# Kernel optimization log

Hardware: AMD Instinct MI355X
Metric: run time of the kernel (lower is better)

Reference implementation:

```python
import jax, jax.numpy as jnp
import numpy as np

N = 500000   # num_nodes
B = 512      # batch_size
D = 128      # node_dim
G = 128      # global_dim
MC = 64      # max_cubes
M = 24       # max_moves_per_cube
H = 128      # MLP hidden
NEG = -1000000000.0


def setup_inputs() -> dict:
    key = jax.random.key(0)
    ks = jax.random.split(key, 8)
    node_features = jax.random.normal(ks[0], (N, D), jnp.float32)
    global_features = jax.random.normal(ks[1], (B, G), jnp.float32)
    cube_mask = jax.random.randint(ks[2], (N,), 0, 2) == 1
    batch = jnp.sort(jax.random.randint(ks[3], (N,), 0, B))
    move_mask = jax.random.randint(ks[4], (B, MC, M), 0, 2) == 1
    W1 = jax.random.normal(ks[5], (D + G, H), jnp.float32) * 0.05
    b1 = jnp.zeros((H,), jnp.float32)
    W2 = jax.random.normal(ks[6], (H, M), jnp.float32) * 0.05
    b2 = jnp.zeros((M,), jnp.float32)
    return {"node_features": node_features, "global_features": global_features,
            "W1": W1, "b1": b1, "W2": W2, "b2": b2,
            "cube_mask": cube_mask, "batch": batch, "move_mask": move_mask}


def reference(node_features, global_features, W1, b1, W2, b2, cube_mask, batch, move_mask):
    bsz = global_features.shape[0]
    max_cubes, moves = move_mask.shape[1], move_mask.shape[2]
    batch = batch.astype(jnp.int32)

    # gather global features per node, concat, small MLP (scores computed for all
    # nodes; only cube-node rows are ever scattered, matching the original math)
    combined = jnp.concatenate([node_features, global_features[batch]], axis=-1)  # [N, D+G]
    h = jax.nn.relu(combined @ W1 + b1)                                           # [N, H]
    scores = h @ W2 + b2                                                          # [N, M]

    # per-batch cumulative cube count (batch is sorted): cube_idx_in_batch
    mask_i = cube_mask.astype(jnp.int32)
    cum = jnp.cumsum(mask_i)                                   # inclusive prefix count of cubes
    counts = jax.ops.segment_sum(mask_i, batch, num_segments=bsz)
    offsets = jnp.concatenate([jnp.zeros((1,), jnp.int32),
                               jnp.cumsum(counts)[:-1].astype(jnp.int32)])
    cube_idx = cum - 1 - offsets[batch]                        # index of cube within its graph

    valid = cube_mask & (cube_idx < max_cubes)
    ib = jnp.where(valid, batch, bsz)      # out-of-range rows -> dropped
    ic = jnp.where(valid, cube_idx, 0)

    logits = jnp.full((bsz, max_cubes, moves), NEG, dtype=scores.dtype)
    logits = logits.at[ib, ic].set(scores, mode="drop")        # unique (ib, ic) per valid node

    logits_flat = logits.reshape(bsz, -1)
    logits_flat = jnp.where(move_mask.reshape(bsz, -1), logits_flat, NEG)
    return logits_flat
```

## Files before the change

### kernel.cpp

```cpp
#include <hip/hip_runtime.h>

typedef short bf16x8 __attribute__((ext_vector_type(8)));
typedef float f32x4 __attribute__((ext_vector_type(4)));

#define NEGV -1000000000.0f

__device__ __forceinline__ unsigned short f2bf(float f) {
    unsigned int u = __float_as_uint(f);
    u += 0x7FFFu + ((u >> 16) & 1u);
    return (unsigned short)(u >> 16);
}

__global__ void prep_kernel(const float* __restrict__ W1, const float* __restrict__ W2,
                            const int* __restrict__ batch, int N, int B,
                            int* __restrict__ batch_start,
                            unsigned short* __restrict__ w1t, unsigned short* __restrict__ w2t) {
    int idx = blockIdx.x * 256 + threadIdx.x;
    if (idx < N) {
        int bcur = batch[idx];
        if (idx == 0) {
            for (int bb = 0; bb <= bcur; ++bb) batch_start[bb] = 0;
        } else {
            int bprev = batch[idx - 1];
            for (int bb = bprev + 1; bb <= bcur; ++bb) batch_start[bb] = idx;
        }
        if (idx == N - 1) {
            for (int bb = bcur + 1; bb <= B; ++bb) batch_start[bb] = N;
        }
    }
    if (idx < 128 * 256) {
        int col = idx >> 8, k = idx & 255;
        w1t[col * 256 + k] = f2bf(W1[k * 128 + col]);
    }
    if (idx < 32 * 128) {
        int col = idx >> 7, k = idx & 127;
        w2t[col * 128 + k] = (col < 24) ? f2bf(W2[k * 24 + col]) : (unsigned short)0;
    }
}

__global__ void __launch_bounds__(256, 2)
fused_kernel(const float* __restrict__ nf, const float* __restrict__ gf,
             const unsigned short* __restrict__ w1t, const unsigned short* __restrict__ w2t,
             const float* __restrict__ b1, const float* __restrict__ b2,
             const int* __restrict__ cube_mask, const int* __restrict__ batch_start,
             const int* __restrict__ move_mask, float* __restrict__ out, int N) {
    __shared__ __align__(16) char smem[(64 * 72 + 128 * 72) * 2 * 2];
    __shared__ __align__(16) unsigned short ldsW2[32][136];
    __shared__ int lds_node[64];
    __shared__ int wt[4];
    unsigned short (*ldsA0)[72]  = (unsigned short (*)[72])smem;
    unsigned short (*ldsB0)[72]  = (unsigned short (*)[72])(smem + 9216);
    unsigned short (*ldsA1)[72]  = (unsigned short (*)[72])(smem + 27648);
    unsigned short (*ldsB1)[72]  = (unsigned short (*)[72])(smem + 27648 + 9216);
    unsigned short (*ldsH)[136]  = (unsigned short (*)[136])smem;

    int t = threadIdx.x;
    int blk = blockIdx.x;
    int lane = t & 63, w = t >> 6;
    int wm = w >> 1, wn = w & 1;
    int r = t >> 2, q = t & 3;
    int bcol = t >> 1, bh0 = (t & 1) * 32;

    int segs = batch_start[blk], sege = batch_start[blk + 1];

    if (t < 64) lds_node[t] = -1;

    int w2col = t >> 3, w2k0 = (t & 7) * 16;
    bf16x8 w2a, w2b;
    {
        const unsigned short* src = w2t + w2col * 128 + w2k0;
        w2a = *(const bf16x8*)(src);
        w2b = *(const bf16x8*)(src + 8);
    }
    bf16x8 fB[4];
#define LOAD_W1(ch) do {                                                         \
        const unsigned short* srcB = w1t + bcol * 256 + (ch) * 64 + bh0;         \
        fB[0] = *(const bf16x8*)(srcB);      fB[1] = *(const bf16x8*)(srcB + 8); \
        fB[2] = *(const bf16x8*)(srcB + 16); fB[3] = *(const bf16x8*)(srcB + 24);\
    } while (0)
    LOAD_W1(2);
    float4 fGl[4], fGh[4];
    {
        const float* srcG = gf + (size_t)blk * 128 + q * 16;
#pragma unroll
        for (int i = 0; i < 4; ++i) {
            fGl[i] = *(const float4*)(srcG + i * 4);
            fGh[i] = *(const float4*)(srcG + 64 + i * 4);
        }
    }
    float b1v[4];
#pragma unroll
    for (int nt = 0; nt < 4; ++nt) b1v[nt] = b1[wn * 64 + nt * 16 + (lane & 15)];
    float b2v[2];
    int mmv[8];
#pragma unroll
    for (int ct = 0; ct < 2; ++ct) {
        int m = ct * 16 + (lane & 15);
        if (m < 24) {
            b2v[ct] = b2[m];
#pragma unroll
            for (int rr = 0; rr < 4; ++rr) {
                int row = w * 16 + (lane >> 4) * 4 + rr;
                mmv[ct * 4 + rr] = move_mask[(size_t)(blk * 64 + row) * 24 + m];
            }
        } else {
            b2v[ct] = 0.f;
#pragma unroll
            for (int rr = 0; rr < 4; ++rr) mmv[ct * 4 + rr] = 0;
        }
    }

    int base = segs & ~3;
    if (base > N - 1024) base = (N - 1024) & ~3;
    int4 cmv = *(const int4*)(cube_mask + base + t * 4);

#define STAGE_A(AB, s0, s1, s2, s3) do {                                         \
        unsigned short tmp[16];                                                  \
        tmp[0]  = f2bf((s0).x); tmp[1]  = f2bf((s0).y); tmp[2]  = f2bf((s0).z); tmp[3]  = f2bf((s0).w); \
        tmp[4]  = f2bf((s1).x); tmp[5]  = f2bf((s1).y); tmp[6]  = f2bf((s1).z); tmp[7]  = f2bf((s1).w); \
        tmp[8]  = f2bf((s2).x); tmp[9]  = f2bf((s2).y); tmp[10] = f2bf((s2).z); tmp[11] = f2bf((s2).w); \
        tmp[12] = f2bf((s3).x); tmp[13] = f2bf((s3).y); tmp[14] = f2bf((s3).z); tmp[15] = f2bf((s3).w); \
        *(bf16x8*)&AB[r][q * 16]     = *(bf16x8*)&tmp[0];                        \
        *(bf16x8*)&AB[r][q * 16 + 8] = *(bf16x8*)&tmp[8];                        \
    } while (0)
#define STAGE_B(BB) do {                                                         \
        *(bf16x8*)&BB[bcol][bh0]      = fB[0];                                   \
        *(bf16x8*)&BB[bcol][bh0 + 8]  = fB[1];                                   \
        *(bf16x8*)&BB[bcol][bh0 + 16] = fB[2];                                   \
        *(bf16x8*)&BB[bcol][bh0 + 24] = fB[3];                                   \
    } while (0)
#define MFMA_CHUNK(AA, BB) do {                                                  \
        _Pragma("unroll")                                                        \
        for (int ks = 0; ks < 2; ++ks) {                                         \
            int ko = ks * 32 + (lane >> 4) * 8;                                  \
            bf16x8 af[2], bfr[4];                                                \
            _Pragma("unroll")                                                    \
            for (int mt = 0; mt < 2; ++mt)                                       \
                af[mt] = *(const bf16x8*)&AA[wm * 32 + mt * 16 + (lane & 15)][ko]; \
            _Pragma("unroll")                                                    \
            for (int nt = 0; nt < 4; ++nt)                                       \
                bfr[nt] = *(const bf16x8*)&BB[wn * 64 + nt * 16 + (lane & 15)][ko]; \
            _Pragma("unroll")                                                    \
            for (int mt = 0; mt < 2; ++mt)                                       \
                _Pragma("unroll")                                                \
                for (int nt = 0; nt < 4; ++nt)                                   \
                    acc[mt][nt] = __builtin_amdgcn_mfma_f32_16x16x32_bf16(       \
                        af[mt], bfr[nt], acc[mt][nt], 0, 0, 0);                  \
        }                                                                        \
    } while (0)

    *(bf16x8*)&ldsW2[w2col][w2k0]     = w2a;
    *(bf16x8*)&ldsW2[w2col][w2k0 + 8] = w2b;
    STAGE_A(ldsA0, fGl[0], fGl[1], fGl[2], fGl[3]);
    STAGE_B(ldsB0);
    LOAD_W1(3);

    f32x4 acc[2][4];
#pragma unroll
    for (int i = 0; i < 2; ++i)
#pragma unroll
        for (int j = 0; j < 4; ++j) acc[i][j] = (f32x4){0.f, 0.f, 0.f, 0.f};

    __syncthreads();

    STAGE_A(ldsA1, fGh[0], fGh[1], fGh[2], fGh[3]);
    STAGE_B(ldsB1);
    LOAD_W1(0);

    int c_t = 0;
#pragma unroll
    for (int j = 0; j < 4; ++j) {
        int i = base + t * 4 + j;
        int mk = ((const int*)&cmv)[j];
        c_t += (i >= segs && i < sege && mk != 0) ? 1 : 0;
    }
    int inc = c_t;
#pragma unroll
    for (int d = 1; d < 64; d <<= 1) {
        int o = __shfl_up(inc, d);
        if (lane >= d) inc += o;
    }
    if (lane == 63) wt[w] = inc;

    MFMA_CHUNK(ldsA0, ldsB0);
    __syncthreads();

    int waveOfs = 0, total = 0;
#pragma unroll
    for (int j = 0; j < 4; ++j) { int c = wt[j]; if (j < w) waveOfs += c; total += c; }
    {
        int rank = waveOfs + (inc - c_t);
#pragma unroll
        for (int j = 0; j < 4; ++j) {
            int i = base + t * 4 + j;
            int mk = ((const int*)&cmv)[j];
            if (i >= segs && i < sege && mk != 0) {
                if (rank < 64) lds_node[rank] = i;
                ++rank;
            }
        }
    }
    int found = total;
    for (int pos = base + 1024; pos < sege && found < 64; pos += 256) {
        int i = pos + t;
        int mk = (i < sege) ? cube_mask[i] : 0;
        unsigned long long bal = __ballot(mk != 0);
        int below = __popcll(bal & ((1ULL << lane) - 1ULL));
        __syncthreads();
        if (lane == 0) wt[w] = __popcll(bal);
        __syncthreads();
        int wofs = 0, tot = 0;
#pragma unroll
        for (int j = 0; j < 4; ++j) { int c = wt[j]; if (j < w) wofs += c; tot += c; }
        int rk = found + wofs + below;
        if (mk && rk < 64) lds_node[rk] = i;
        found += tot;
    }
    __syncthreads();

    int n = lds_node[r];
    int nrow = (n >= 0) ? n : 0;
    const float* srcN = nf + (size_t)nrow * 128 + q * 16;
    float4 fN[8];
#pragma unroll
    for (int i = 0; i < 4; ++i) {
        fN[i]     = *(const float4*)(srcN + i * 4);
        fN[4 + i] = *(const float4*)(srcN + 64 + i * 4);
    }

    MFMA_CHUNK(ldsA1, ldsB1);
    STAGE_B(ldsB0);
    LOAD_W1(1);
    STAGE_A(ldsA0, fN[0], fN[1], fN[2], fN[3]);
    __syncthreads();

    MFMA_CHUNK(ldsA0, ldsB0);
    STAGE_A(ldsA1, fN[4], fN[5], fN[6], fN[7]);
    STAGE_B(ldsB1);
    __syncthreads();

    MFMA_CHUNK(ldsA1, ldsB1);

#undef STAGE_A
#undef STAGE_B
#undef LOAD_W1
#undef MFMA_CHUNK

#pragma unroll
    for (int nt = 0; nt < 4; ++nt) {
        int col = wn * 64 + nt * 16 + (lane & 15);
        float bias = b1v[nt];
#pragma unroll
        for (int mt = 0; mt < 2; ++mt) {
            int row0 = wm * 32 + mt * 16 + (lane >> 4) * 4;
#pragma unroll
            for (int rr = 0; rr < 4; ++rr) {
                float v = acc[mt][nt][rr] + bias;
                v = v > 0.f ? v : 0.f;
                ldsH[row0 + rr][col] = f2bf(v);
            }
        }
    }
    __syncthreads();

    f32x4 acc2[2];
    acc2[0] = (f32x4){0.f, 0.f, 0.f, 0.f};
    acc2[1] = (f32x4){0.f, 0.f, 0.f, 0.f};
#pragma unroll
    for (int ks = 0; ks < 4; ++ks) {
        int ko = ks * 32 + (lane >> 4) * 8;
        bf16x8 a2 = *(const bf16x8*)&ldsH[w * 16 + (lane & 15)][ko];
#pragma unroll
        for (int ct = 0; ct < 2; ++ct) {
            bf16x8 bw = *(const bf16x8*)&ldsW2[ct * 16 + (lane & 15)][ko];
            acc2[ct] = __builtin_amdgcn_mfma_f32_16x16x32_bf16(a2, bw, acc2[ct], 0, 0, 0);
        }
    }

#pragma unroll
    for (int ct = 0; ct < 2; ++ct) {
        int m = ct * 16 + (lane & 15);
        if (m >= 24) continue;
#pragma unroll
        for (int rr = 0; rr < 4; ++rr) {
            int row = w * 16 + (lane >> 4) * 4 + rr;
            size_t oidx = (size_t)(blk * 64 + row) * 24 + m;
            float v = acc2[ct][rr] + b2v[ct];
            bool keep = (lds_node[row] >= 0) && (mmv[ct * 4 + rr] != 0);
            out[oidx] = keep ? v : NEGV;
        }
    }
}

extern "C" void kernel_launch(void* const* d_in, const int* in_sizes, int n_in,
                              void* d_out, int out_size, void* d_ws, size_t ws_size,
                              hipStream_t stream) {
    const float* nf = (const float*)d_in[0];
    const float* gf = (const float*)d_in[1];
    const float* W1 = (const float*)d_in[2];
    const float* b1 = (const float*)d_in[3];
    const float* W2 = (const float*)d_in[4];
    const float* b2 = (const float*)d_in[5];
    const int* cube_mask = (const int*)d_in[6];
    const int* batch     = (const int*)d_in[7];
    const int* move_mask = (const int*)d_in[8];
    float* out = (float*)d_out;

    int N = in_sizes[6];
    int B = in_sizes[1] / 128;

    char* ws = (char*)d_ws;
    int* batch_start = (int*)(ws);
    unsigned short* w1t = (unsigned short*)(ws + 4096);
    unsigned short* w2t = (unsigned short*)(ws + 69632);

    int NB = (N + 255) / 256;
    prep_kernel<<<NB, 256, 0, stream>>>(W1, W2, batch, N, B, batch_start, w1t, w2t);
    fused_kernel<<<B, 256, 0, stream>>>(nf, gf, w1t, w2t, b1, b2,
                                        cube_mask, batch_start, move_mask, out, N);
    (void)n_in; (void)out_size; (void)ws_size;
}
```

Baseline: 18.40 us.

## Speculatively prefetch cube_mask window and vectorize batch_start prep

The fused kernel no longer waits for batch_start before loading cube_mask. It guesses where each graph's segment starts from a uniform-distribution estimate, loads a 3584-entry cube_mask window into LDS straight away, and falls back to a global load if the real segment lies outside that window. The aim is to take a dependent global-load latency off the kernel's critical path, at the cost of extra LDS use and wasted bandwidth. Separately, the prep kernel now handles four batch entries per thread with a vector load, which cuts its launch to a quarter of the blocks.

```diff
diff --git a/kernel.cpp b/kernel.cpp
--- a/kernel.cpp
+++ b/kernel.cpp
@@ -4,6 +4,7 @@
 typedef float f32x4 __attribute__((ext_vector_type(4)));
 
 #define NEGV -1000000000.0f
+#define WINI 3584
 
 __device__ __forceinline__ unsigned short f2bf(float f) {
     unsigned int u = __float_as_uint(f);
@@ -16,16 +17,20 @@
                             int* __restrict__ batch_start,
                             unsigned short* __restrict__ w1t, unsigned short* __restrict__ w2t) {
     int idx = blockIdx.x * 256 + threadIdx.x;
-    if (idx < N) {
-        int bcur = batch[idx];
-        if (idx == 0) {
-            for (int bb = 0; bb <= bcur; ++bb) batch_start[bb] = 0;
-        } else {
-            int bprev = batch[idx - 1];
-            for (int bb = bprev + 1; bb <= bcur; ++bb) batch_start[bb] = idx;
-        }
-        if (idx == N - 1) {
-            for (int bb = bcur + 1; bb <= B; ++bb) batch_start[bb] = N;
+    int i0 = idx * 4;
+    if (i0 < N) {
+        int4 v = *(const int4*)(batch + i0);
+        int prev = (i0 == 0) ? -1 : batch[i0 - 1];
+        const int* vv = (const int*)&v;
+#pragma unroll
+        for (int j = 0; j < 4; ++j) {
+            int i = i0 + j;
+            if (i < N) {
+                int b = vv[j];
+                if (b != prev) { for (int bb = prev + 1; bb <= b; ++bb) batch_start[bb] = i; }
+                if (i == N - 1) { for (int bb = b + 1; bb <= B; ++bb) batch_start[bb] = N; }
+                prev = b;
+            }
         }
     }
     if (idx < 128 * 256) {
@@ -43,9 +48,10 @@
              const unsigned short* __restrict__ w1t, const unsigned short* __restrict__ w2t,
              const float* __restrict__ b1, const float* __restrict__ b2,
              const int* __restrict__ cube_mask, const int* __restrict__ batch_start,
-             const int* __restrict__ move_mask, float* __restrict__ out, int N) {
+             const int* __restrict__ move_mask, float* __restrict__ out, int N, int B) {
     __shared__ __align__(16) char smem[(64 * 72 + 128 * 72) * 2 * 2];
     __shared__ __align__(16) unsigned short ldsW2[32][136];
+    __shared__ __align__(16) int ldsWin[WINI];
     __shared__ int lds_node[64];
     __shared__ int wt[4];
     unsigned short (*ldsA0)[72]  = (unsigned short (*)[72])smem;
@@ -62,6 +68,20 @@
     int bcol = t >> 1, bh0 = (t & 1) * 32;
 
     int segs = batch_start[blk], sege = batch_start[blk + 1];
+
+    int est = (int)(((long long)blk * N) / B);
+    int wstart = est - 1280;
+    if (wstart < 0) wstart = 0;
+    if (wstart > N - WINI) wstart = N - WINI;
+    wstart &= ~3;
+    int4 wv4[3];
+    int2 wv2;
+    {
+        const int* wsrc = cube_mask + wstart;
+#pragma unroll
+        for (int j = 0; j < 3; ++j) wv4[j] = *(const int4*)(wsrc + j * 1024 + t * 4);
+        wv2 = *(const int2*)(wsrc + 3072 + t * 2);
+    }
 
     if (t < 64) lds_node[t] = -1;
 
@@ -110,9 +130,9 @@
         }
     }
 
-    int base = segs & ~3;
-    if (base > N - 1024) base = (N - 1024) & ~3;
-    int4 cmv = *(const int4*)(cube_mask + base + t * 4);
+#pragma unroll
+    for (int j = 0; j < 3; ++j) *(int4*)&ldsWin[j * 1024 + t * 4] = wv4[j];
+    *(int2*)&ldsWin[3072 + t * 2] = wv2;
 
 #define STAGE_A(AB, s0, s1, s2, s3) do {                                         \
         unsigned short tmp[16];                                                  \
@@ -163,6 +183,16 @@
 
     __syncthreads();
 
+    int base = segs & ~3;
+    if (base > N - 1024) base = (N - 1024) & ~3;
+    int off = base - wstart;
+    int4 cmv;
+    if (off >= 0 && off <= WINI - 1024) {
+        cmv = *(const int4*)&ldsWin[off + t * 4];
+    } else {
+        cmv = *(const int4*)(cube_mask + base + t * 4);
+    }
+
     STAGE_A(ldsA1, fGh[0], fGh[1], fGh[2], fGh[3]);
     STAGE_B(ldsB1);
     LOAD_W1(0);
@@ -314,9 +344,9 @@
     unsigned short* w1t = (unsigned short*)(ws + 4096);
     unsigned short* w2t = (unsigned short*)(ws + 69632);
 
-    int NB = (N + 255) / 256;
+    int NB = (N + 1023) / 1024;
     prep_kernel<<<NB, 256, 0, stream>>>(W1, W2, batch, N, B, batch_start, w1t, w2t);
     fused_kernel<<<B, 256, 0, stream>>>(nf, gf, w1t, w2t, b1, b2,
-                                        cube_mask, batch_start, move_mask, out, N);
+                                        cube_mask, batch_start, move_mask, out, N, B);
     (void)n_in; (void)out_size; (void)ws_size;
 }
```

Measured after the change: 19.49 us. +5.9%, slower.
